# Performance work log

Measured on AMD Instinct MI355X. Metric: run time of the kernel, lower is better.

The kernel has to match this reference:

```python
import jax, jax.numpy as jnp
import numpy as np

B, S, H, D = 2, 2048, 16, 64
E = H * D
ROPE_BASE = 10000.0


def rotate_half(x):
    x1 = x[..., ::2]
    x2 = x[..., 1::2]
    return jnp.concatenate((-x2, x1), axis=-1)


def rope_embeddings(seq_len, head_dim, base):
    inv_freq = 1.0 / base ** (jnp.arange(0, head_dim, 2, dtype=jnp.float32) / head_dim)
    pos = jnp.arange(seq_len, dtype=jnp.float32)
    freqs = jnp.outer(pos, inv_freq)  # (S, D/2)
    emb = jnp.concatenate((freqs, freqs), axis=-1)  # (S, D)
    return jnp.cos(emb)[None, :, None, :], jnp.sin(emb)[None, :, None, :]


def setup_inputs() -> dict:
    key = jax.random.key(0)
    ks = jax.random.split(key, 5)
    x = jax.random.normal(ks[0], (B, S, E), dtype=jnp.float32)
    # causal boolean mask: True = masked (disallowed)
    mask = ~jnp.tril(jnp.ones((S, S), dtype=bool))[None, None]
    scale = 1.0 / np.sqrt(E)
    Wq = jax.random.normal(ks[1], (E, E), dtype=jnp.float32) * scale
    Wk = jax.random.normal(ks[2], (E, E), dtype=jnp.float32) * scale
    Wv = jax.random.normal(ks[3], (E, E), dtype=jnp.float32) * scale
    Wo = jax.random.normal(ks[4], (E, E), dtype=jnp.float32) * scale
    return {"x": x, "mask": mask, "Wq": Wq, "Wk": Wk, "Wv": Wv, "Wo": Wo}


def reference(x, mask, Wq, Wk, Wv, Wo):
    b, s, e = x.shape
    q = (x @ Wq).reshape(b, s, H, D)
    k = (x @ Wk).reshape(b, s, H, D)
    v = (x @ Wv).reshape(b, s, H, D)
    cos_emb, sin_emb = rope_embeddings(s, D, ROPE_BASE)
    q = q * cos_emb + rotate_half(q) * sin_emb
    k = k * cos_emb + rotate_half(k) * sin_emb
    # (b, h, s_q, s_k)
    scores = jnp.einsum('bqhd,bkhd->bhqk', q, k) / jnp.sqrt(jnp.float32(D))
    mask_b = jnp.broadcast_to(mask, (b, H, s, s))
    scores = jnp.where(mask_b, jnp.finfo(jnp.float32).min, scores)
    attn = jax.nn.softmax(scores, axis=-1)
    out = jnp.einsum('bhqk,bkhd->bqhd', attn, v).reshape(b, s, e)
    return out @ Wo
```

## Files before the change

kernel.cpp:

```cpp
#include <hip/hip_runtime.h>

#define SEQ 2048
#define NH 16
#define HD 64
#define EMB 1024

typedef __attribute__((ext_vector_type(4))) float f32x4;
typedef __attribute__((ext_vector_type(16))) float f32x16;
typedef __attribute__((ext_vector_type(8))) __bf16 bf16x8;
typedef unsigned int u32x2 __attribute__((ext_vector_type(2)));
typedef unsigned int u32x4 __attribute__((ext_vector_type(4)));

__device__ inline unsigned short f2bf(float f){
  unsigned int u = __float_as_uint(f);
  return (unsigned short)((u + 0x7fffu + ((u >> 16) & 1u)) >> 16);
}
__device__ inline float bf2f(unsigned short h){ return __uint_as_float(((unsigned int)h) << 16); }

__device__ inline unsigned cvtpk(float lo, float hi){
  unsigned r;
  asm("v_cvt_pk_bf16_f32 %0, %1, %2" : "=v"(r) : "v"(lo), "v"(hi));
  return r;
}
__device__ inline u32x2 plswap(unsigned a, unsigned b){
  return __builtin_amdgcn_permlane32_swap(a, b, false, false);
}
__device__ inline float exp2a(float x){
  float r;
  asm("v_exp_f32 %0, %1" : "=v"(r) : "v"(x));
  return r;
}

__global__ __launch_bounds__(256) void k_prep(const float* __restrict__ xin,
                                              unsigned short* __restrict__ xb,
                                              const float* __restrict__ Wq, const float* __restrict__ Wk,
                                              const float* __restrict__ Wv, const float* __restrict__ Wo,
                                              unsigned short* __restrict__ WtQKV,
                                              unsigned short* __restrict__ WtO,
                                              float2* __restrict__ tb){
  int bid = blockIdx.x;
  int tid = threadIdx.x;
  if (bid < 2048){
    int i = bid * 256 + tid;
    const float4* p = (const float4*)xin + (size_t)i * 2;
    float4 a = p[0], b = p[1];
    uint4 r;
    r.x = f2bf(a.x) | ((unsigned)f2bf(a.y) << 16);
    r.y = f2bf(a.z) | ((unsigned)f2bf(a.w) << 16);
    r.z = f2bf(b.x) | ((unsigned)f2bf(b.y) << 16);
    r.w = f2bf(b.z) | ((unsigned)f2bf(b.w) << 16);
    ((uint4*)xb)[i] = r;
  } else if (bid < 6144){
    int rb = bid - 2048;
    int z = rb >> 10, rem = rb & 1023;
    const float* W = (z == 0) ? Wq : (z == 1) ? Wk : (z == 2) ? Wv : Wo;
    unsigned short* out = (z < 3) ? (WtQKV + (size_t)z * EMB * EMB) : WtO;
    __shared__ float t[32][33];
    int n0 = (rem & 31) * 32, k0 = (rem >> 5) * 32;
    int tx = tid & 31, ty = tid >> 5;
    #pragma unroll
    for (int i = 0; i < 4; ++i)
      t[ty + i * 8][tx] = W[(size_t)(k0 + ty + i * 8) * EMB + n0 + tx];
    __syncthreads();
    #pragma unroll
    for (int i = 0; i < 4; ++i)
      out[(size_t)(n0 + ty + i * 8) * EMB + k0 + tx] = f2bf(t[tx][ty + i * 8]);
  } else {
    int idx = (bid - 6144) * 256 + tid;
    int s = idx >> 5, j = idx & 31;
    float invf = __expf(-(float)j * (9.210340371976184f / 32.0f));
    float ang = (float)s * invf;
    tb[idx] = make_float2(cosf(ang), sinf(ang));
  }
}

template<int MODE>
__global__ __launch_bounds__(256, MODE == 0 ? 3 : 2) void k_gemm(
                                                 const unsigned short* __restrict__ A,
                                                 const unsigned short* __restrict__ Bt,
                                                 unsigned short* __restrict__ Qf,
                                                 unsigned short* __restrict__ Kf,
                                                 unsigned short* __restrict__ Vf,
                                                 float* __restrict__ FO,
                                                 const float2* __restrict__ tb){
  const int Kd = 1024;
  int m0 = blockIdx.x * 128, n0 = blockIdx.y * 128;
  int tid = threadIdx.x;
  int w = tid >> 6, lane = tid & 63;
  int wm = w >> 1, wn = w & 1;
  int g = lane >> 4, lr = lane & 15;
  __shared__ __align__(16) unsigned char shm[43008];
  unsigned short* Ash = (unsigned short*)shm;
  unsigned short* Bsh = (unsigned short*)(shm + 16384);
  f32x4 acc[4][4] = {};
  int r_ = tid >> 3, c_ = tid & 7;
  int rm = r_ & 7;
  int cc = c_ ^ rm;
  for (int kt = 0; kt < Kd / 64; ++kt){
    int kb = kt * 64;
    #pragma unroll
    for (int it = 0; it < 4; ++it){
      int row = it * 32 + r_;
      __builtin_amdgcn_global_load_lds(
        (const __attribute__((address_space(1))) void*)(A + (size_t)(m0 + row) * Kd + kb + cc * 8),
        (__attribute__((address_space(3))) void*)(Ash + it * 2048 + tid * 8), 16, 0, 0);
      __builtin_amdgcn_global_load_lds(
        (const __attribute__((address_space(1))) void*)(Bt + (size_t)(n0 + row) * Kd + kb + cc * 8),
        (__attribute__((address_space(3))) void*)(Bsh + it * 2048 + tid * 8), 16, 0, 0);
    }
    __syncthreads();
    #pragma unroll
    for (int kk = 0; kk < 2; ++kk){
      bf16x8 af[4], bfr[4];
      #pragma unroll
      for (int i = 0; i < 4; ++i){
        int ra = wm * 64 + i * 16 + lr;
        af[i]  = *(const bf16x8*)(Ash + ra * 64 + (((kk * 4 + g) ^ (ra & 7)) * 8));
        int rb = wn * 64 + i * 16 + lr;
        bfr[i] = *(const bf16x8*)(Bsh + rb * 64 + (((kk * 4 + g) ^ (rb & 7)) * 8));
      }
      #pragma unroll
      for (int mi = 0; mi < 4; ++mi)
        #pragma unroll
        for (int ni = 0; ni < 4; ++ni)
          acc[mi][ni] = __builtin_amdgcn_mfma_f32_16x16x32_bf16(af[mi], bfr[ni], acc[mi][ni], 0, 0, 0);
    }
    __syncthreads();
  }

  if constexpr (MODE == 1){
    float* tf = (float*)(shm + w * 10752);
    #pragma unroll
    for (int mi = 0; mi < 4; ++mi){
      __syncthreads();
      #pragma unroll
      for (int ni = 0; ni < 4; ++ni)
        #pragma unroll
        for (int r = 0; r < 4; ++r)
          tf[(4 * g + r) * 64 + ni * 16 + lr] = acc[mi][ni][r];
      __syncthreads();
      #pragma unroll
      for (int it = 0; it < 4; ++it){
        int chunk = it * 64 + lane;
        int rr = chunk >> 4, c4 = chunk & 15;
        float4 v = *(float4*)&tf[rr * 64 + c4 * 4];
        int mrow = m0 + wm * 64 + mi * 16 + rr;
        *(float4*)&FO[(size_t)mrow * EMB + n0 + wn * 64 + c4 * 4] = v;
      }
    }
  } else {
    unsigned char* tile = shm + w * 10752;
    int mat = n0 >> 10;
    float scl = (mat == 0) ? 0.18033688011112042f : 1.0f;
    #pragma unroll
    for (int mi = 0; mi < 4; ++mi)
      #pragma unroll
      for (int ni = 0; ni < 4; ++ni)
        #pragma unroll
        for (int r = 0; r < 4; ++r)
          *(unsigned short*)(tile + (mi * 16 + 4 * g + r) * 168 + (ni * 16 + lr) * 2)
              = f2bf(acc[mi][ni][r] * scl);
    __syncthreads();
    int l32 = lane & 31, h2 = lane >> 5;
    int rowbase = m0 + wm * 64;
    int bb = rowbase >> 11, sbase = rowbase & 2047;
    int hd = ((n0 & 1023) >> 6) + wn;
    size_t tbase = (size_t)((bb * NH + hd) * 64 + (sbase >> 5));
    if (mat < 2){
      unsigned short* dst = mat ? Kf : Qf;
      #pragma unroll
      for (int tt = 0; tt < 2; ++tt){
        int srow = sbase + tt * 32 + l32;
        const unsigned char* base = tile + (tt * 32 + l32) * 168;
        #pragma unroll
        for (int d0 = 0; d0 < 4; ++d0){
          bf16x8 own = *(const bf16x8*)(base + d0 * 32 + h2 * 16);
          bf16x8 plo = *(const bf16x8*)(base + (d0 & 1) * 64 + h2 * 32);
          bf16x8 phi = *(const bf16x8*)(base + (d0 & 1) * 64 + h2 * 32 + 16);
          bf16x8 part = (d0 < 2)
            ? __builtin_shufflevector(plo, phi, 1, 3, 5, 7, 9, 11, 13, 15)
            : __builtin_shufflevector(plo, phi, 0, 2, 4, 6, 8, 10, 12, 14);
          const float4* cp = (const float4*)(tb + (size_t)srow * 32 + (d0 & 1) * 16 + h2 * 8);
          float4 c0 = cp[0], c1 = cp[1], c2 = cp[2], c3 = cp[3];
          float co[8] = {c0.x, c0.z, c1.x, c1.z, c2.x, c2.z, c3.x, c3.z};
          float si[8] = {c0.y, c0.w, c1.y, c1.w, c2.y, c2.w, c3.y, c3.w};
          float sg = (d0 < 2) ? -1.0f : 1.0f;
          unsigned wv[4];
          #pragma unroll
          for (int i2 = 0; i2 < 4; ++i2){
            float e0 = (float)own[2 * i2]     * co[2 * i2]     + sg * (float)part[2 * i2]     * si[2 * i2];
            float e1 = (float)own[2 * i2 + 1] * co[2 * i2 + 1] + sg * (float)part[2 * i2 + 1] * si[2 * i2 + 1];
            wv[i2] = (unsigned)f2bf(e0) | ((unsigned)f2bf(e1) << 16);
          }
          uint4 o; o.x = wv[0]; o.y = wv[1]; o.z = wv[2]; o.w = wv[3];
          ((uint4*)dst)[((tbase + tt) * 4 + d0) * 64 + lane] = o;
        }
      }
    } else {
      #pragma unroll
      for (int tt = 0; tt < 2; ++tt)
        #pragma unroll
        for (int dt = 0; dt < 2; ++dt)
          #pragma unroll
          for (int s2 = 0; s2 < 2; ++s2){
            unsigned wv[4];
            #pragma unroll
            for (int i2 = 0; i2 < 4; ++i2){
              unsigned a = *(const unsigned short*)(tile + (tt * 32 + s2 * 16 + h2 * 8 + 2 * i2) * 168 + (dt * 32 + l32) * 2);
              unsigned b = *(const unsigned short*)(tile + (tt * 32 + s2 * 16 + h2 * 8 + 2 * i2 + 1) * 168 + (dt * 32 + l32) * 2);
              wv[i2] = a | (b << 16);
            }
            uint4 o; o.x = wv[0]; o.y = wv[1]; o.z = wv[2]; o.w = wv[3];
            ((uint4*)Vf)[((tbase + tt) * 4 + dt * 2 + s2) * 64 + lane] = o;
          }
    }
  }
}

#define MBIAS 8.0f

__global__ __launch_bounds__(128, 2) void k_attn(const unsigned short* __restrict__ Qf,
                                                 const unsigned short* __restrict__ Kf,
                                                 const unsigned short* __restrict__ Vf,
                                                 unsigned short* __restrict__ AO){
  int b0 = blockIdx.x;
  int bh = (b0 & 7) + 8 * (b0 >> 8);
  int p  = (b0 >> 3) & 31;
  int jA = p, jB = 63 - p;
  int q0A = jA * 32, q0B = jB * 32;
  int wid = threadIdx.x >> 6;
  int l = threadIdx.x & 63;
  int lr = l & 31, h = l >> 5;
  const unsigned short* Kp = Kf + (size_t)bh * 64 * 4 * 512;
  const unsigned short* Vp = Vf + (size_t)bh * 64 * 4 * 512;

  bf16x8 qfA[4], qfB[4];
  #pragma unroll
  for (int d0 = 0; d0 < 4; ++d0){
    qfA[d0] = *(const bf16x8*)(Qf + ((size_t)(bh * 64 + jA) * 4 + d0) * 512 + l * 8);
    qfB[d0] = *(const bf16x8*)(Qf + ((size_t)(bh * 64 + jB) * 4 + d0) * 512 + l * 8);
  }

  bf16x8 kf0[4], kf1[4], vf0[2][2], vf1[2][2];

  f32x16 oA0 = {}, oA1 = {}, oB0 = {}, oB1 = {};
  float lA = 0.f, lB = 0.f;

  auto LOADT = [&](bf16x8 (&kb)[4], bf16x8 (&vb)[2][2], int tt){
    const unsigned short* Kn = Kp + (size_t)tt * 4 * 512;
    const unsigned short* Vn = Vp + (size_t)tt * 4 * 512;
    #pragma unroll
    for (int d0 = 0; d0 < 4; ++d0)
      kb[d0] = *(const bf16x8*)(Kn + (size_t)d0 * 512 + l * 8);
    #pragma unroll
    for (int dt = 0; dt < 2; ++dt)
      #pragma unroll
      for (int s = 0; s < 2; ++s)
        vb[dt][s] = *(const bf16x8*)(Vn + (size_t)(dt * 2 + s) * 512 + l * 8);
  };

  auto PROC = [&](const bf16x8 (&kb)[4], const bf16x8 (&vb)[2][2], int tt){
    bool actA = (tt <= jA);
    __builtin_amdgcn_s_setprio(1);
    f32x16 stB, stA;
    #pragma unroll
    for (int r = 0; r < 16; ++r) stB[r] = -MBIAS;
    #pragma unroll
    for (int d0 = 0; d0 < 4; ++d0)
      stB = __builtin_amdgcn_mfma_f32_32x32x16_bf16(kb[d0], qfB[d0], stB, 0, 0, 0);
    if (actA){
      #pragma unroll
      for (int r = 0; r < 16; ++r) stA[r] = -MBIAS;
      #pragma unroll
      for (int d0 = 0; d0 < 4; ++d0)
        stA = __builtin_amdgcn_mfma_f32_32x32x16_bf16(kb[d0], qfA[d0], stA, 0, 0, 0);
    }
    __builtin_amdgcn_s_setprio(0);

    if (tt == jB){
      #pragma unroll
      for (int r = 0; r < 16; ++r){
        int kkl = (r & 3) + 8 * (r >> 2) + 4 * h;
        if (kkl > lr) stB[r] = -3.0e38f;
      }
    }
    #pragma unroll
    for (int r = 0; r < 16; ++r) stB[r] = exp2a(stB[r]);
    {
      float s8[8];
      #pragma unroll
      for (int r = 0; r < 8; ++r) s8[r] = stB[r] + stB[r + 8];
      #pragma unroll
      for (int r = 0; r < 4; ++r) s8[r] += s8[r + 4];
      lB += (s8[0] + s8[1]) + (s8[2] + s8[3]);
    }
    bf16x8 pfB[2];
    #pragma unroll
    for (int s = 0; s < 2; ++s){
      unsigned c0 = cvtpk(stB[8 * s + 0], stB[8 * s + 1]);
      unsigned c1 = cvtpk(stB[8 * s + 2], stB[8 * s + 3]);
      unsigned c2 = cvtpk(stB[8 * s + 4], stB[8 * s + 5]);
      unsigned c3 = cvtpk(stB[8 * s + 6], stB[8 * s + 7]);
      u32x2 r02 = plswap(c0, c2);
      u32x2 r13 = plswap(c1, c3);
      u32x4 uw;
      uw.x = r02.x; uw.y = r13.x; uw.z = r02.y; uw.w = r13.y;
      pfB[s] = __builtin_bit_cast(bf16x8, uw);
    }
    __builtin_amdgcn_s_setprio(1);
    #pragma unroll
    for (int s = 0; s < 2; ++s){
      oB0 = __builtin_amdgcn_mfma_f32_32x32x16_bf16(vb[0][s], pfB[s], oB0, 0, 0, 0);
      oB1 = __builtin_amdgcn_mfma_f32_32x32x16_bf16(vb[1][s], pfB[s], oB1, 0, 0, 0);
    }
    __builtin_amdgcn_s_setprio(0);

    if (actA){
      if (tt == jA){
        #pragma unroll
        for (int r = 0; r < 16; ++r){
          int kkl = (r & 3) + 8 * (r >> 2) + 4 * h;
          if (kkl > lr) stA[r] = -3.0e38f;
        }
      }
      #pragma unroll
      for (int r = 0; r < 16; ++r) stA[r] = exp2a(stA[r]);
      {
        float s8[8];
        #pragma unroll
        for (int r = 0; r < 8; ++r) s8[r] = stA[r] + stA[r + 8];
        #pragma unroll
        for (int r = 0; r < 4; ++r) s8[r] += s8[r + 4];
        lA += (s8[0] + s8[1]) + (s8[2] + s8[3]);
      }
      bf16x8 pfA[2];
      #pragma unroll
      for (int s = 0; s < 2; ++s){
        unsigned c0 = cvtpk(stA[8 * s + 0], stA[8 * s + 1]);
        unsigned c1 = cvtpk(stA[8 * s + 2], stA[8 * s + 3]);
        unsigned c2 = cvtpk(stA[8 * s + 4], stA[8 * s + 5]);
        unsigned c3 = cvtpk(stA[8 * s + 6], stA[8 * s + 7]);
        u32x2 r02 = plswap(c0, c2);
        u32x2 r13 = plswap(c1, c3);
        u32x4 uw;
        uw.x = r02.x; uw.y = r13.x; uw.z = r02.y; uw.w = r13.y;
        pfA[s] = __builtin_bit_cast(bf16x8, uw);
      }
      __builtin_amdgcn_s_setprio(1);
      #pragma unroll
      for (int s = 0; s < 2; ++s){
        oA0 = __builtin_amdgcn_mfma_f32_32x32x16_bf16(vb[0][s], pfA[s], oA0, 0, 0, 0);
        oA1 = __builtin_amdgcn_mfma_f32_32x32x16_bf16(vb[1][s], pfA[s], oA1, 0, 0, 0);
      }
      __builtin_amdgcn_s_setprio(0);
    }
  };

  LOADT(kf0, vf0, wid);
  for (int t = wid; t <= jB; t += 4){
    int t2 = (t + 2 > jB) ? jB : t + 2;
    LOADT(kf1, vf1, t2);
    PROC(kf0, vf0, t);
    int t4 = (t + 4 > jB) ? jB : t + 4;
    LOADT(kf0, vf0, t4);
    if (t + 2 <= jB) PROC(kf1, vf1, t + 2);
  }

  __shared__ float xch[66 * 64];
  if (wid == 1){
    #pragma unroll
    for (int r = 0; r < 16; ++r) xch[r * 64 + l]        = oA0[r];
    #pragma unroll
    for (int r = 0; r < 16; ++r) xch[(16 + r) * 64 + l] = oA1[r];
    #pragma unroll
    for (int r = 0; r < 16; ++r) xch[(32 + r) * 64 + l] = oB0[r];
    #pragma unroll
    for (int r = 0; r < 16; ++r) xch[(48 + r) * 64 + l] = oB1[r];
    xch[64 * 64 + l] = lA;
    xch[65 * 64 + l] = lB;
  }
  __syncthreads();
  if (wid == 0){
    #pragma unroll
    for (int r = 0; r < 16; ++r){
      oA0[r] += xch[r * 64 + l];
      oA1[r] += xch[(16 + r) * 64 + l];
      oB0[r] += xch[(32 + r) * 64 + l];
      oB1[r] += xch[(48 + r) * 64 + l];
    }
    lA += xch[64 * 64 + l];
    lB += xch[65 * 64 + l];

    int b = bh >> 4, hh = bh & 15;
    {
      u32x2 ss = plswap(__float_as_uint(lA), __float_as_uint(lA));
      float inv = 1.0f / (__uint_as_float(ss.x) + __uint_as_float(ss.y));
      unsigned short* outp = AO + ((size_t)(b * SEQ + q0A + lr)) * EMB + hh * HD;
      #pragma unroll
      for (int rq = 0; rq < 4; ++rq){
        uint2 wv;
        wv.x = cvtpk(oA0[rq * 4 + 0] * inv, oA0[rq * 4 + 1] * inv);
        wv.y = cvtpk(oA0[rq * 4 + 2] * inv, oA0[rq * 4 + 3] * inv);
        *(uint2*)(outp + 8 * rq + 4 * h) = wv;
      }
      #pragma unroll
      for (int rq = 0; rq < 4; ++rq){
        uint2 wv;
        wv.x = cvtpk(oA1[rq * 4 + 0] * inv, oA1[rq * 4 + 1] * inv);
        wv.y = cvtpk(oA1[rq * 4 + 2] * inv, oA1[rq * 4 + 3] * inv);
        *(uint2*)(outp + 32 + 8 * rq + 4 * h) = wv;
      }
    }
    {
      u32x2 ss = plswap(__float_as_uint(lB), __float_as_uint(lB));
      float inv = 1.0f / (__uint_as_float(ss.x) + __uint_as_float(ss.y));
      unsigned short* outp = AO + ((size_t)(b * SEQ + q0B + lr)) * EMB + hh * HD;
      #pragma unroll
      for (int rq = 0; rq < 4; ++rq){
        uint2 wv;
        wv.x = cvtpk(oB0[rq * 4 + 0] * inv, oB0[rq * 4 + 1] * inv);
        wv.y = cvtpk(oB0[rq * 4 + 2] * inv, oB0[rq * 4 + 3] * inv);
        *(uint2*)(outp + 8 * rq + 4 * h) = wv;
      }
      #pragma unroll
      for (int rq = 0; rq < 4; ++rq){
        uint2 wv;
        wv.x = cvtpk(oB1[rq * 4 + 0] * inv, oB1[rq * 4 + 1] * inv);
        wv.y = cvtpk(oB1[rq * 4 + 2] * inv, oB1[rq * 4 + 3] * inv);
        *(uint2*)(outp + 32 + 8 * rq + 4 * h) = wv;
      }
    }
  }
}

extern "C" void kernel_launch(void* const* d_in, const int* in_sizes, int n_in,
                              void* d_out, int out_size, void* d_ws, size_t ws_size,
                              hipStream_t stream){
  const float* x  = (const float*)d_in[0];
  const float* Wq = (const float*)d_in[2];
  const float* Wk = (const float*)d_in[3];
  const float* Wv = (const float*)d_in[4];
  const float* Wo = (const float*)d_in[5];
  float* out = (float*)d_out;

  char* ws = (char*)d_ws;
  size_t off = 0;
  auto alloc = [&](size_t bytes){ void* p = ws + off; off += (bytes + 255) & ~(size_t)255; return p; };
  unsigned short* xb    = (unsigned short*)alloc((size_t)4096 * 1024 * 2);
  unsigned short* wtqkv = (unsigned short*)alloc((size_t)3072 * 1024 * 2);
  unsigned short* wto   = (unsigned short*)alloc((size_t)1024 * 1024 * 2);
  float2*         tb    = (float2*)alloc((size_t)2048 * 32 * 8);
  unsigned short* Qf    = (unsigned short*)alloc((size_t)4096 * 1024 * 2);
  unsigned short* Kf    = (unsigned short*)alloc((size_t)4096 * 1024 * 2);
  unsigned short* Vf    = (unsigned short*)alloc((size_t)4096 * 1024 * 2);
  unsigned short* ao = xb;

  k_prep<<<dim3(6400), dim3(256), 0, stream>>>(x, xb, Wq, Wk, Wv, Wo, wtqkv, wto, tb);
  k_gemm<0><<<dim3(32, 24), dim3(256), 0, stream>>>(xb, wtqkv, Qf, Kf, Vf, nullptr, tb);
  k_attn<<<dim3(1024), dim3(128), 0, stream>>>(Qf, Kf, Vf, ao);
  k_gemm<1><<<dim3(32, 8), dim3(256), 0, stream>>>(ao, wto, nullptr, nullptr, nullptr, out, nullptr);
}
```

Baseline: 90.00 us.

## Split attention KV tiles across four waves per block instead of two

The attention kernel now launches 256 threads (four waves) per block. Each wave handles every fourth KV tile, with double-buffered loads striding by eight, and the four partial outputs are reduced through a larger shared-memory exchange buffer. This cuts the serial KV loop length per wave and adds latency-hiding parallelism for each query-pair block. In exchange it uses more LDS (about 50KB), does more reduction work at the end, and may lower occupancy under launch_bounds(256,2).

After: 89.97 us (median of 2 runs). Within noise of the previous version (-0.0%).

```diff
diff --git a/kernel.cpp b/kernel.cpp
--- a/kernel.cpp
+++ b/kernel.cpp
@@ -219,7 +219,7 @@
 
 #define MBIAS 8.0f
 
-__global__ __launch_bounds__(128, 2) void k_attn(const unsigned short* __restrict__ Qf,
+__global__ __launch_bounds__(256, 2) void k_attn(const unsigned short* __restrict__ Qf,
                                                  const unsigned short* __restrict__ Kf,
                                                  const unsigned short* __restrict__ Vf,
                                                  unsigned short* __restrict__ AO){
@@ -357,39 +357,44 @@
   };
 
   LOADT(kf0, vf0, wid);
-  for (int t = wid; t <= jB; t += 4){
-    int t2 = (t + 2 > jB) ? jB : t + 2;
-    LOADT(kf1, vf1, t2);
+  for (int t = wid; t <= jB; t += 8){
+    int t1 = (t + 4 > jB) ? jB : t + 4;
+    LOADT(kf1, vf1, t1);
     PROC(kf0, vf0, t);
-    int t4 = (t + 4 > jB) ? jB : t + 4;
-    LOADT(kf0, vf0, t4);
-    if (t + 2 <= jB) PROC(kf1, vf1, t + 2);
-  }
-
-  __shared__ float xch[66 * 64];
-  if (wid == 1){
-    #pragma unroll
-    for (int r = 0; r < 16; ++r) xch[r * 64 + l]        = oA0[r];
-    #pragma unroll
-    for (int r = 0; r < 16; ++r) xch[(16 + r) * 64 + l] = oA1[r];
-    #pragma unroll
-    for (int r = 0; r < 16; ++r) xch[(32 + r) * 64 + l] = oB0[r];
-    #pragma unroll
-    for (int r = 0; r < 16; ++r) xch[(48 + r) * 64 + l] = oB1[r];
-    xch[64 * 64 + l] = lA;
-    xch[65 * 64 + l] = lB;
+    int t2 = (t + 8 > jB) ? jB : t + 8;
+    LOADT(kf0, vf0, t2);
+    if (t + 4 <= jB) PROC(kf1, vf1, t + 4);
+  }
+
+  __shared__ float xch[3][66 * 64];
+  if (wid >= 1){
+    float* xs = xch[wid - 1];
+    #pragma unroll
+    for (int r = 0; r < 16; ++r) xs[r * 64 + l]        = oA0[r];
+    #pragma unroll
+    for (int r = 0; r < 16; ++r) xs[(16 + r) * 64 + l] = oA1[r];
+    #pragma unroll
+    for (int r = 0; r < 16; ++r) xs[(32 + r) * 64 + l] = oB0[r];
+    #pragma unroll
+    for (int r = 0; r < 16; ++r) xs[(48 + r) * 64 + l] = oB1[r];
+    xs[64 * 64 + l] = lA;
+    xs[65 * 64 + l] = lB;
   }
   __syncthreads();
   if (wid == 0){
     #pragma unroll
-    for (int r = 0; r < 16; ++r){
-      oA0[r] += xch[r * 64 + l];
-      oA1[r] += xch[(16 + r) * 64 + l];
-      oB0[r] += xch[(32 + r) * 64 + l];
-      oB1[r] += xch[(48 + r) * 64 + l];
-    }
-    lA += xch[64 * 64 + l];
-    lB += xch[65 * 64 + l];
+    for (int s = 0; s < 3; ++s){
+      const float* xs = xch[s];
+      #pragma unroll
+      for (int r = 0; r < 16; ++r){
+        oA0[r] += xs[r * 64 + l];
+        oA1[r] += xs[(16 + r) * 64 + l];
+        oB0[r] += xs[(32 + r) * 64 + l];
+        oB1[r] += xs[(48 + r) * 64 + l];
+      }
+      lA += xs[64 * 64 + l];
+      lB += xs[65 * 64 + l];
+    }
 
     int b = bh >> 4, hh = bh & 15;
     {
@@ -457,6 +462,6 @@
 
   k_prep<<<dim3(6400), dim3(256), 0, stream>>>(x, xb, Wq, Wk, Wv, Wo, wtqkv, wto, tb);
   k_gemm<0><<<dim3(32, 24), dim3(256), 0, stream>>>(xb, wtqkv, Qf, Kf, Vf, nullptr, tb);
-  k_attn<<<dim3(1024), dim3(128), 0, stream>>>(Qf, Kf, Vf, ao);
+  k_attn<<<dim3(1024), dim3(256), 0, stream>>>(Qf, Kf, Vf, ao);
   k_gemm<1><<<dim3(32, 8), dim3(256), 0, stream>>>(ao, wto, nullptr, nullptr, nullptr, out, nullptr);
 }
```
